# Performance work log

Measured on AMD Instinct MI355X. Metric: run time of the kernel, lower is better.

Reference implementation:

```python
import jax, jax.numpy as jnp
import numpy as np

B, N, D, H, C = 32, 128, 5000, 256, 4  # trees, nodes/tree, input_size_rumor, hidden, rumor_classes


def setup_inputs() -> dict:
    key = jax.random.key(0)
    ks = jax.random.split(key, 24)
    scale = 0.05  # xavier-like scale (module calls init_weight with xavier_uniform_)
    inp = {"x": jax.random.normal(ks[0], (B, N, D), dtype=jnp.float32)}
    names = ["Er", "Wsr_r", "Usr_r", "Wsr_z", "Usr_z", "Wsr_h", "Usr_h",
             "Wr_r", "Ur_r", "Usr2r_r", "Wr_z", "Ur_z", "Usr2r_z",
             "Wr_h", "Ur_h", "Usr2r_h"]
    shapes = [(H, D)] + [(H, H)] * 15
    for i, (n, s) in enumerate(zip(names, shapes)):
        inp[n] = jax.random.normal(ks[i + 1], s, dtype=jnp.float32) * scale
    inp["Vr"] = jax.random.normal(ks[17], (C, H), dtype=jnp.float32) * scale
    inp["br"] = jnp.zeros((C, 1), dtype=jnp.float32)
    # Tree structure: nodes in topological order; slot 0 = zero initial state,
    # node j is stored at slot j+1, parents[:, i] is the SLOT of node i's parent.
    rng = np.random.default_rng(0)
    pslot = np.zeros((B, N), dtype=np.int64)  # root's parent slot = 0 (zeros)
    for i in range(1, N):
        pslot[:, i] = rng.integers(1, i + 1, size=B)  # parent is an earlier node
    has_child = np.zeros((B, N), dtype=bool)
    for i in range(1, N):
        has_child[np.arange(B), pslot[:, i] - 1] = True
    inp["parents"] = jnp.asarray(pslot)
    inp["is_leaf"] = jnp.asarray(~has_child)
    return inp


def _tree_gru(x_tilde, parents, Wsr_r, Usr_r, Wsr_z, Usr_z, Wsr_h, Usr_h,
              Wr_r, Ur_r, Usr2r_r, Wr_z, Ur_z, Usr2r_z, Wr_h, Ur_h, Usr2r_h):
    """x_tilde: [B,N,H] embedded node features; parents: [B,N] parent SLOT ids.
    Returns h_rumor for every node: [B,N,H]. Same math as MultiModel.rumor_forward,
    with the Python recursion replaced by a scan over topologically-ordered nodes,
    vectorized across the batch of trees."""
    Bq, Nq, Hq = x_tilde.shape
    S0 = jnp.zeros((Bq, Nq + 1, Hq), x_tilde.dtype)  # slot 0 = initial zero state

    def step(carry, xs):
        S_sh, S_ru = carry  # [B, N+1, H] stored shared/rumor states
        xt, p, i = xs       # xt: [B,H], p: [B] parent slot, i: node index
        idx = p[:, None, None]
        hsp = jnp.take_along_axis(S_sh, idx, axis=1)[:, 0]  # [B,H] parent shared state
        hrp = jnp.take_along_axis(S_ru, idx, axis=1)[:, 0]  # [B,H] parent rumor state
        # shared GRU cell
        r_sh = jax.nn.sigmoid(xt @ Wsr_r.T + hsp @ Usr_r.T)
        z_sh = jax.nn.sigmoid(xt @ Wsr_z.T + hsp @ Usr_z.T)
        h_sh_t = jnp.tanh(xt @ Wsr_h.T + (hsp * r_sh) @ Usr_h.T)
        h_sh = (1 - z_sh) * hsp + z_sh * h_sh_t
        # rumor GRU cell (conditioned on shared state)
        r_ru = jax.nn.sigmoid(xt @ Wr_r.T + hrp @ Ur_r.T + h_sh @ Usr2r_r.T)
        z_ru = jax.nn.sigmoid(xt @ Wr_z.T + hrp @ Ur_z.T + h_sh @ Usr2r_z.T)
        h_ru_t = jnp.tanh(xt @ Wr_h.T + (hrp * r_ru) @ Ur_h.T + h_sh @ Usr2r_h.T)
        h_ru = (1 - z_ru) * hrp + z_ru * h_ru_t
        S_sh = S_sh.at[:, i + 1, :].set(h_sh)
        S_ru = S_ru.at[:, i + 1, :].set(h_ru)
        return (S_sh, S_ru), None

    xs = (jnp.swapaxes(x_tilde, 0, 1), parents.T, jnp.arange(Nq))
    (S_sh, S_ru), _ = jax.lax.scan(step, (S0, S0), xs)
    return S_ru[:, 1:, :]


def reference(x, Er, Wsr_r, Usr_r, Wsr_z, Usr_z, Wsr_h, Usr_h,
              Wr_r, Ur_r, Usr2r_r, Wr_z, Ur_z, Usr2r_z, Wr_h, Ur_h, Usr2r_h,
              Vr, br, parents, is_leaf):
    x_tilde = jnp.einsum('bnd,hd->bnh', x, Er)  # Er @ x for every node
    H_ru = _tree_gru(x_tilde, parents, Wsr_r, Usr_r, Wsr_z, Usr_z, Wsr_h, Usr_h,
                     Wr_r, Ur_r, Usr2r_r, Wr_z, Ur_z, Usr2r_z, Wr_h, Ur_h, Usr2r_h)
    # max over leaf node hidden vectors (torch.max over cat of leaf vectors)
    neg = jnp.finfo(H_ru.dtype).min
    hmax = jnp.where(is_leaf[:, :, None], H_ru, neg).max(axis=1)  # [B,H]
    logits = hmax @ Vr.T + br[:, 0]  # [B,C]
    return jax.nn.softmax(logits, axis=-1)
```

## Files before the change

### kernel.cpp

```cpp
#include <hip/hip_runtime.h>
#include <hip/hip_bf16.h>
#include <math.h>


#define H_DIM 256
#define N_NODES 128
#define B_TREES 32
#define MAXL 128
#define TPB 4
#define GRID_WGS 256

typedef short bf16x8 __attribute__((ext_vector_type(8)));
typedef float f32x4 __attribute__((ext_vector_type(4)));

__device__ __forceinline__ float sigmoidf_(float x) {
    return 1.0f / (1.0f + expf(-x));
}
__device__ __forceinline__ unsigned bfp(float x) {
    unsigned u = __float_as_uint(x);
    return (u + 0x7fffu + ((u >> 16) & 1u)) >> 16;
}
__device__ __forceinline__ float bflo(unsigned w) { return __uint_as_float(w << 16); }
__device__ __forceinline__ float bfhi(unsigned w) { return __uint_as_float(w & 0xffff0000u); }

__device__ __forceinline__ void unpack8(uint4 v, float* f) {
    f[0] = bflo(v.x); f[1] = bfhi(v.x);
    f[2] = bflo(v.y); f[3] = bfhi(v.y);
    f[4] = bflo(v.z); f[5] = bfhi(v.z);
    f[6] = bflo(v.w); f[7] = bfhi(v.w);
}

__device__ __forceinline__ float coh_load(const float* p) {
    return __hip_atomic_load(p, __ATOMIC_RELAXED, __HIP_MEMORY_SCOPE_AGENT);
}
__device__ __forceinline__ void coh_store(float* p, float v) {
    __hip_atomic_store(p, v, __ATOMIC_RELAXED, __HIP_MEMORY_SCOPE_AGENT);
}
__device__ __forceinline__ unsigned coh_loadu(const unsigned* p) {
    return __hip_atomic_load(p, __ATOMIC_RELAXED, __HIP_MEMORY_SCOPE_AGENT);
}
__device__ __forceinline__ void coh_storeu(unsigned* p, unsigned v) {
    __hip_atomic_store(p, v, __ATOMIC_RELAXED, __HIP_MEMORY_SCOPE_AGENT);
}

__global__ __launch_bounds__(256) void gemm_mfma_nt(
    const float* __restrict__ A, const float* __restrict__ B,
    float* __restrict__ C, int K, int ldc) {
    __shared__ short As[64][40];
    __shared__ short Bs[64][40];
    const int tid = threadIdx.x;
    const int bm = blockIdx.x, bn = blockIdx.y;
    const int row = tid >> 2;
    const int quad = tid & 3;
    const int wave = tid >> 6;
    const int lane = tid & 63;
    const int lm = lane & 15;
    const int kq = lane >> 4;

    f32x4 acc[4];
#pragma unroll
    for (int i = 0; i < 4; ++i) acc[i] = (f32x4){0.f, 0.f, 0.f, 0.f};

    const int nk = (K + 31) >> 5;
    for (int kt = 0; kt < nk; ++kt) {
        const int k0 = kt << 5;
        const int kbase = k0 + quad * 8;
        {
            float a8[8];
            const float* Ap = A + (size_t)(bm * 64 + row) * K + kbase;
            if (kbase + 8 <= K) {
                const float4 v0 = *(const float4*)Ap;
                const float4 v1 = *(const float4*)(Ap + 4);
                a8[0] = v0.x; a8[1] = v0.y; a8[2] = v0.z; a8[3] = v0.w;
                a8[4] = v1.x; a8[5] = v1.y; a8[6] = v1.z; a8[7] = v1.w;
            } else {
#pragma unroll
                for (int i = 0; i < 8; ++i)
                    a8[i] = (kbase + i < K) ? Ap[i] : 0.f;
            }
            uint4 v;
            v.x = bfp(a8[0]) | (bfp(a8[1]) << 16);
            v.y = bfp(a8[2]) | (bfp(a8[3]) << 16);
            v.z = bfp(a8[4]) | (bfp(a8[5]) << 16);
            v.w = bfp(a8[6]) | (bfp(a8[7]) << 16);
            *(uint4*)&As[row][quad * 8] = v;
        }
        {
            float b8[8];
            const float* Bp = B + (size_t)(bn * 64 + row) * K + kbase;
            if (kbase + 8 <= K) {
                const float4 v0 = *(const float4*)Bp;
                const float4 v1 = *(const float4*)(Bp + 4);
                b8[0] = v0.x; b8[1] = v0.y; b8[2] = v0.z; b8[3] = v0.w;
                b8[4] = v1.x; b8[5] = v1.y; b8[6] = v1.z; b8[7] = v1.w;
            } else {
#pragma unroll
                for (int i = 0; i < 8; ++i)
                    b8[i] = (kbase + i < K) ? Bp[i] : 0.f;
            }
            uint4 v;
            v.x = bfp(b8[0]) | (bfp(b8[1]) << 16);
            v.y = bfp(b8[2]) | (bfp(b8[3]) << 16);
            v.z = bfp(b8[4]) | (bfp(b8[5]) << 16);
            v.w = bfp(b8[6]) | (bfp(b8[7]) << 16);
            *(uint4*)&Bs[row][quad * 8] = v;
        }
        __syncthreads();
        const bf16x8 af = *(const bf16x8*)&As[wave * 16 + lm][kq * 8];
#pragma unroll
        for (int nt = 0; nt < 4; ++nt) {
            const bf16x8 bf = *(const bf16x8*)&Bs[nt * 16 + lm][kq * 8];
            acc[nt] = __builtin_amdgcn_mfma_f32_16x16x32_bf16(af, bf, acc[nt], 0, 0, 0);
        }
        __syncthreads();
    }
#pragma unroll
    for (int nt = 0; nt < 4; ++nt) {
#pragma unroll
        for (int r = 0; r < 4; ++r) {
            const int gm = bm * 64 + wave * 16 + kq * 4 + r;
            const int gn = bn * 64 + nt * 16 + lm;
            C[(size_t)gm * ldc + gn] = acc[nt][r];
        }
    }
}

__global__ __launch_bounds__(256) void transpose_pack_u(
    const float* __restrict__ U0, const float* __restrict__ U1,
    const float* __restrict__ U2, const float* __restrict__ U3,
    const float* __restrict__ U4, const float* __restrict__ U5,
    const float* __restrict__ U6, const float* __restrict__ U7,
    const float* __restrict__ U8, uint4* __restrict__ UTb) {
    const float* Us[9] = {U0, U1, U2, U3, U4, U5, U6, U7, U8};
    const int jb = blockIdx.x;
    const int m = blockIdx.y;
    const int h = threadIdx.x;
    const float* U = Us[m] + (size_t)h * 256 + jb * 8;
    uint4 v;
    v.x = bfp(U[0]) | (bfp(U[1]) << 16);
    v.y = bfp(U[2]) | (bfp(U[3]) << 16);
    v.z = bfp(U[4]) | (bfp(U[5]) << 16);
    v.w = bfp(U[6]) | (bfp(U[7]) << 16);
    UTb[(size_t)(m * 32 + jb) * 256 + h] = v;
}

__global__ __launch_bounds__(256) void build_schedule(
    const int* __restrict__ parents, int* __restrict__ sched,
    int* __restrict__ level_off, int* __restrict__ gstart,
    int* __restrict__ gend, int* __restrict__ ngrp,
    unsigned* __restrict__ ready) {
    __shared__ unsigned char depth[B_TREES][N_NODES];
    __shared__ int counts[MAXL];
    __shared__ int base[MAXL + 1];
    const int tid = threadIdx.x;
    for (int k = tid; k < B_TREES * N_NODES; k += 256)
        coh_storeu(&ready[k], 0u);
    for (int k = tid; k < MAXL; k += 256) counts[k] = 0;
    __syncthreads();
    if (tid < B_TREES) {
        depth[tid][0] = 0;
        for (int i = 1; i < N_NODES; ++i) {
            const int p = parents[tid * N_NODES + i];
            depth[tid][i] = (unsigned char)(depth[tid][p - 1] + 1);
        }
    }
    __syncthreads();
    for (int k = tid; k < B_TREES * N_NODES; k += 256)
        atomicAdd(&counts[depth[k >> 7][k & 127]], 1);
    __syncthreads();
    if (tid == 0) {
        int acc = 0;
        int nl = 0;
        for (int l = 0; l < MAXL; ++l) {
            base[l] = acc;
            acc += counts[l];
            if (counts[l] > 0) nl = l + 1;
        }
        base[MAXL] = acc;
        level_off[MAXL + 1] = nl;
        int ng = 0;
        for (int l = 0; l < nl; ++l) {
            for (int s = base[l]; s < base[l + 1]; s += TPB) {
                gstart[ng] = s;
                gend[ng] = (s + TPB < base[l + 1]) ? s + TPB : base[l + 1];
                ++ng;
            }
        }
        *ngrp = ng;
    }
    __syncthreads();
    for (int k = tid; k <= MAXL; k += 256) level_off[k] = base[k];
    for (int k = tid; k < MAXL; k += 256) counts[k] = 0;
    __syncthreads();
    for (int k = tid; k < B_TREES * N_NODES; k += 256) {
        const int d = depth[k >> 7][k & 127];
        const int pos = base[d] + atomicAdd(&counts[d], 1);
        sched[pos] = k;
    }
}

__global__ __launch_bounds__(256, 1) void tree_scan_df(
    const float* __restrict__ P, const uint4* __restrict__ UTb,
    const int* __restrict__ parents,
    const int* __restrict__ sched,
    const int* __restrict__ gstart, const int* __restrict__ gend,
    const int* __restrict__ ngrp, unsigned* __restrict__ ready,
    float* __restrict__ Ssh, float* __restrict__ Sru) {
    const int h = threadIdx.x;
    const int wg = blockIdx.x;
    __shared__ float hsp_s[H_DIM][TPB];
    __shared__ float hrp_s[H_DIM][TPB];
    __shared__ float aux_s[H_DIM][TPB];
    __shared__ float hsh_s[H_DIM][TPB];

    const uint4* __restrict__ U0b = UTb + 0 * 8192;
    const uint4* __restrict__ U1b = UTb + 1 * 8192;
    const uint4* __restrict__ U2b = UTb + 2 * 8192;
    const uint4* __restrict__ U3b = UTb + 3 * 8192;
    const uint4* __restrict__ U4b = UTb + 4 * 8192;
    const uint4* __restrict__ U5b = UTb + 5 * 8192;
    const uint4* __restrict__ U6b = UTb + 6 * 8192;
    const uint4* __restrict__ U7b = UTb + 7 * 8192;
    const uint4* __restrict__ U8b = UTb + 8 * 8192;

    const int ng = ngrp[0];
    for (int g = wg; g < ng; g += GRID_WGS) {
        const int s = gstart[g];
        const int e = gend[g];
        if (h == 0) {
            for (int i = s; i < e; ++i) {
                const int nd = sched[i];
                const int p = parents[nd];
                if (p != 0) {
                    const unsigned* f = &ready[(nd & ~127) + p - 1];
                    while (coh_loadu(f) == 0u) __builtin_amdgcn_s_sleep(2);
                }
            }
        }
        __syncthreads();

        int  node[TPB];
        bool val[TPB];
        float phs[TPB], phr[TPB];
#pragma unroll
        for (int t = 0; t < TPB; ++t) {
            const int idx = s + t;
            val[t] = idx < e;
            const int nd = val[t] ? sched[idx] : sched[s];
            node[t] = nd;
            const int p = parents[nd];
            float hs = 0.f, hr = 0.f;
            if (p != 0) {
                const size_t pr = ((size_t)((nd & ~127) + p - 1)) * H_DIM + h;
                hs = coh_load(&Ssh[pr]);
                hr = coh_load(&Sru[pr]);
            }
            phs[t] = hs;
            phr[t] = hr;
        }
        *(float4*)&hsp_s[h][0] = make_float4(phs[0], phs[1], phs[2], phs[3]);
        *(float4*)&hrp_s[h][0] = make_float4(phr[0], phr[1], phr[2], phr[3]);
        __syncthreads();

        float pr_[TPB], pz_[TPB];
#pragma unroll
        for (int t = 0; t < TPB; ++t) {
            const float* Pi = P + (size_t)node[t] * 1536;
            pr_[t] = Pi[h];
            pz_[t] = Pi[256 + h];
        }
        float dr[TPB] = {0.f, 0.f, 0.f, 0.f};
        float dz[TPB] = {0.f, 0.f, 0.f, 0.f};
#pragma unroll 4
        for (int jb = 0; jb < 32; ++jb) {
            const uint4 w0 = U0b[jb * 256 + h];
            const uint4 w1 = U1b[jb * 256 + h];
            float a[8], c[8];
            unpack8(w0, a);
            unpack8(w1, c);
#pragma unroll
            for (int q = 0; q < 8; ++q) {
                const float4 hv = *(const float4*)&hsp_s[jb * 8 + q][0];
                const float hv4[4] = {hv.x, hv.y, hv.z, hv.w};
#pragma unroll
                for (int t = 0; t < TPB; ++t) {
                    dr[t] = fmaf(a[q], hv4[t], dr[t]);
                    dz[t] = fmaf(c[q], hv4[t], dz[t]);
                }
            }
        }
        float z_sh[TPB], vsh[TPB];
#pragma unroll
        for (int t = 0; t < TPB; ++t) {
            const float r_sh = sigmoidf_(pr_[t] + dr[t]);
            z_sh[t] = sigmoidf_(pz_[t] + dz[t]);
            vsh[t] = phs[t] * r_sh;
        }
        *(float4*)&aux_s[h][0] = make_float4(vsh[0], vsh[1], vsh[2], vsh[3]);
        __syncthreads();

        float ph_[TPB];
#pragma unroll
        for (int t = 0; t < TPB; ++t)
            ph_[t] = P[(size_t)node[t] * 1536 + 512 + h];
        float dh[TPB] = {0.f, 0.f, 0.f, 0.f};
#pragma unroll 8
        for (int jb = 0; jb < 32; ++jb) {
            const uint4 w2 = U2b[jb * 256 + h];
            float a[8];
            unpack8(w2, a);
#pragma unroll
            for (int q = 0; q < 8; ++q) {
                const float4 hv = *(const float4*)&aux_s[jb * 8 + q][0];
                const float hv4[4] = {hv.x, hv.y, hv.z, hv.w};
#pragma unroll
                for (int t = 0; t < TPB; ++t)
                    dh[t] = fmaf(a[q], hv4[t], dh[t]);
            }
        }
        float hsh[TPB];
#pragma unroll
        for (int t = 0; t < TPB; ++t) {
            const float hsh_t = tanhf(ph_[t] + dh[t]);
            hsh[t] = (1.f - z_sh[t]) * phs[t] + z_sh[t] * hsh_t;
            if (val[t])
                coh_store(&Ssh[(size_t)node[t] * H_DIM + h], hsh[t]);
        }
        *(float4*)&hsh_s[h][0] = make_float4(hsh[0], hsh[1], hsh[2], hsh[3]);
        __syncthreads();

        float pru_[TPB], pzu_[TPB];
#pragma unroll
        for (int t = 0; t < TPB; ++t) {
            const float* Pi = P + (size_t)node[t] * 1536;
            pru_[t] = Pi[768 + h];
            pzu_[t] = Pi[1024 + h];
        }
        float er[TPB] = {0.f, 0.f, 0.f, 0.f};
        float ez[TPB] = {0.f, 0.f, 0.f, 0.f};
        float fr[TPB] = {0.f, 0.f, 0.f, 0.f};
        float fz[TPB] = {0.f, 0.f, 0.f, 0.f};
#pragma unroll 2
        for (int jb = 0; jb < 32; ++jb) {
            const uint4 w3 = U3b[jb * 256 + h];
            const uint4 w4 = U4b[jb * 256 + h];
            const uint4 w6 = U6b[jb * 256 + h];
            const uint4 w7 = U7b[jb * 256 + h];
            float a3[8], a4[8], a6[8], a7[8];
            unpack8(w3, a3);
            unpack8(w4, a4);
            unpack8(w6, a6);
            unpack8(w7, a7);
#pragma unroll
            for (int q = 0; q < 8; ++q) {
                const float4 hr4 = *(const float4*)&hrp_s[jb * 8 + q][0];
                const float4 hs4 = *(const float4*)&hsh_s[jb * 8 + q][0];
                const float hrv[4] = {hr4.x, hr4.y, hr4.z, hr4.w};
                const float hsv[4] = {hs4.x, hs4.y, hs4.z, hs4.w};
#pragma unroll
                for (int t = 0; t < TPB; ++t) {
                    er[t] = fmaf(a3[q], hrv[t], er[t]);
                    ez[t] = fmaf(a4[q], hrv[t], ez[t]);
                    fr[t] = fmaf(a6[q], hsv[t], fr[t]);
                    fz[t] = fmaf(a7[q], hsv[t], fz[t]);
                }
            }
        }
        float z_ru[TPB], v2[TPB];
#pragma unroll
        for (int t = 0; t < TPB; ++t) {
            const float r_ru = sigmoidf_(pru_[t] + er[t] + fr[t]);
            z_ru[t] = sigmoidf_(pzu_[t] + ez[t] + fz[t]);
            v2[t] = phr[t] * r_ru;
        }
        *(float4*)&aux_s[h][0] = make_float4(v2[0], v2[1], v2[2], v2[3]);
        __syncthreads();

        float phu_[TPB];
#pragma unroll
        for (int t = 0; t < TPB; ++t)
            phu_[t] = P[(size_t)node[t] * 1536 + 1280 + h];
        float eh[TPB] = {0.f, 0.f, 0.f, 0.f};
        float fh[TPB] = {0.f, 0.f, 0.f, 0.f};
#pragma unroll 4
        for (int jb = 0; jb < 32; ++jb) {
            const uint4 w5 = U5b[jb * 256 + h];
            const uint4 w8 = U8b[jb * 256 + h];
            float a5[8], a8[8];
            unpack8(w5, a5);
            unpack8(w8, a8);
#pragma unroll
            for (int q = 0; q < 8; ++q) {
                const float4 v4 = *(const float4*)&aux_s[jb * 8 + q][0];
                const float4 s4 = *(const float4*)&hsh_s[jb * 8 + q][0];
                const float vv[4] = {v4.x, v4.y, v4.z, v4.w};
                const float sv[4] = {s4.x, s4.y, s4.z, s4.w};
#pragma unroll
                for (int t = 0; t < TPB; ++t) {
                    eh[t] = fmaf(a5[q], vv[t], eh[t]);
                    fh[t] = fmaf(a8[q], sv[t], fh[t]);
                }
            }
        }
#pragma unroll
        for (int t = 0; t < TPB; ++t) {
            const float hru_t = tanhf(phu_[t] + eh[t] + fh[t]);
            const float h_ru = (1.f - z_ru[t]) * phr[t] + z_ru[t] * hru_t;
            if (val[t])
                coh_store(&Sru[(size_t)node[t] * H_DIM + h], h_ru);
        }
        __syncthreads();
        if (h < TPB && s + h < e)
            coh_storeu(&ready[sched[s + h]], 1u);
        __syncthreads();
    }
}

__global__ __launch_bounds__(256) void epilogue_k(
    const float* __restrict__ Sru, const int* __restrict__ is_leaf,
    const float* __restrict__ Vr, const float* __restrict__ br,
    float* __restrict__ out) {
    const int b = blockIdx.x;
    const int h = threadIdx.x;
    float m = -3.402823466e38f;
    for (int n = 0; n < N_NODES; ++n) {
        const float v = Sru[((size_t)b * N_NODES + n) * H_DIM + h];
        if (is_leaf[b * N_NODES + n] != 0) m = fmaxf(m, v);
    }
    __shared__ float hm[H_DIM];
    __shared__ float lg[4];
    hm[h] = m;
    __syncthreads();
    if (h < 4) {
        float acc = br[h];
#pragma unroll 8
        for (int j = 0; j < H_DIM; ++j) acc = fmaf(Vr[h * 256 + j], hm[j], acc);
        lg[h] = acc;
    }
    __syncthreads();
    if (h == 0) {
        const float mx = fmaxf(fmaxf(lg[0], lg[1]), fmaxf(lg[2], lg[3]));
        const float e0 = expf(lg[0] - mx);
        const float e1 = expf(lg[1] - mx);
        const float e2 = expf(lg[2] - mx);
        const float e3 = expf(lg[3] - mx);
        const float s = e0 + e1 + e2 + e3;
        out[b * 4 + 0] = e0 / s;
        out[b * 4 + 1] = e1 / s;
        out[b * 4 + 2] = e2 / s;
        out[b * 4 + 3] = e3 / s;
    }
}

extern "C" void kernel_launch(void* const* d_in, const int* in_sizes, int n_in,
                              void* d_out, int out_size, void* d_ws, size_t ws_size,
                              hipStream_t stream) {
    const float* x      = (const float*)d_in[0];
    const float* Er     = (const float*)d_in[1];
    const float* Wsr_r  = (const float*)d_in[2];
    const float* Usr_r  = (const float*)d_in[3];
    const float* Wsr_z  = (const float*)d_in[4];
    const float* Usr_z  = (const float*)d_in[5];
    const float* Wsr_h  = (const float*)d_in[6];
    const float* Usr_h  = (const float*)d_in[7];
    const float* Wr_r   = (const float*)d_in[8];
    const float* Ur_r   = (const float*)d_in[9];
    const float* Usr2r_r= (const float*)d_in[10];
    const float* Wr_z   = (const float*)d_in[11];
    const float* Ur_z   = (const float*)d_in[12];
    const float* Usr2r_z= (const float*)d_in[13];
    const float* Wr_h   = (const float*)d_in[14];
    const float* Ur_h   = (const float*)d_in[15];
    const float* Usr2r_h= (const float*)d_in[16];
    const float* Vr     = (const float*)d_in[17];
    const float* br     = (const float*)d_in[18];
    const int*   parents= (const int*)d_in[19];
    const int*   is_leaf= (const int*)d_in[20];
    float* out = (float*)d_out;

    float* ws = (float*)d_ws;
    float* xt   = ws;
    float* P    = xt + 1048576;
    float* Wcat = P + 6291456;
    uint4* UTb  = (uint4*)(Wcat + 393216);
    float* Ssh  = (float*)(UTb + 73728);
    float* Sru  = Ssh + 1048576;
    int*   sched     = (int*)(Sru + 1048576);
    int*   level_off = sched + 4096;
    unsigned* ready  = (unsigned*)(level_off + 192);
    int*   gstart    = (int*)(ready + 4096);
    int*   gend      = gstart + 2048;
    int*   ngrp      = gend + 2048;

    dim3 blk(256);

    gemm_mfma_nt<<<dim3(64, 4), blk, 0, stream>>>(x, Er, xt, 5000, 256);

    const float* Ws6[6] = {Wsr_r, Wsr_z, Wsr_h, Wr_r, Wr_z, Wr_h};
    for (int w = 0; w < 6; ++w)
        (void)hipMemcpyAsync(Wcat + (size_t)w * 65536, Ws6[w],
                             65536 * sizeof(float), hipMemcpyDeviceToDevice,
                             stream);
    gemm_mfma_nt<<<dim3(64, 24), blk, 0, stream>>>(xt, Wcat, P, 256, 1536);

    transpose_pack_u<<<dim3(32, 9), blk, 0, stream>>>(
        Usr_r, Usr_z, Usr_h, Ur_r, Ur_z, Ur_h, Usr2r_r, Usr2r_z, Usr2r_h, UTb);

    build_schedule<<<dim3(1), blk, 0, stream>>>(parents, sched, level_off,
                                                gstart, gend, ngrp, ready);

    void* args[] = {(void*)&P, (void*)&UTb, (void*)&parents, (void*)&sched,
                    (void*)&gstart, (void*)&gend, (void*)&ngrp, (void*)&ready,
                    (void*)&Ssh, (void*)&Sru};
    (void)hipLaunchCooperativeKernel((const void*)tree_scan_df,
                                     dim3(GRID_WGS), blk, args, 0, stream);

    epilogue_k<<<dim3(B_TREES), blk, 0, stream>>>(Sru, is_leaf, Vr, br, out);
}
```

Before: 992.0 us.

## Split-K the embedding GEMM, halve nodes per group, parallelize dependency waits

The x·Erᵀ GEMM is split four ways along K (5000), with each slice written to scratch and then summed by a new reduce kernel. This raises the block count from 256 to 1024 on a GEMM that previously ran only 64x4 blocks. The tree scan now packs two nodes per workgroup group instead of four, giving more and smaller groups so the dependency chain is shorter and more parallel. Each node's parent-ready flag is now spun on by its own thread with a shorter sleep. The costs are an extra partial-sum pass through memory and reloading the U weights for fewer nodes per group.

```diff
diff --git a/kernel.cpp b/kernel.cpp
--- a/kernel.cpp
+++ b/kernel.cpp
@@ -7,7 +7,7 @@
 #define N_NODES 128
 #define B_TREES 32
 #define MAXL 128
-#define TPB 4
+#define TPB 2
 #define GRID_WGS 256
 
 typedef short bf16x8 __attribute__((ext_vector_type(8)));
@@ -45,11 +45,15 @@
 
 __global__ __launch_bounds__(256) void gemm_mfma_nt(
     const float* __restrict__ A, const float* __restrict__ B,
-    float* __restrict__ C, int K, int ldc) {
+    float* __restrict__ C, int K, int ldc, int Kc, int zStride) {
     __shared__ short As[64][40];
     __shared__ short Bs[64][40];
     const int tid = threadIdx.x;
     const int bm = blockIdx.x, bn = blockIdx.y;
+    const int z = blockIdx.z;
+    const int k_begin = z * Kc;
+    const int k_end = (k_begin + Kc < K) ? (k_begin + Kc) : K;
+    float* Cz = C + (size_t)z * zStride;
     const int row = tid >> 2;
     const int quad = tid & 3;
     const int wave = tid >> 6;
@@ -61,14 +65,12 @@
 #pragma unroll
     for (int i = 0; i < 4; ++i) acc[i] = (f32x4){0.f, 0.f, 0.f, 0.f};
 
-    const int nk = (K + 31) >> 5;
-    for (int kt = 0; kt < nk; ++kt) {
-        const int k0 = kt << 5;
+    for (int k0 = k_begin; k0 < k_end; k0 += 32) {
         const int kbase = k0 + quad * 8;
         {
             float a8[8];
             const float* Ap = A + (size_t)(bm * 64 + row) * K + kbase;
-            if (kbase + 8 <= K) {
+            if (kbase + 8 <= k_end) {
                 const float4 v0 = *(const float4*)Ap;
                 const float4 v1 = *(const float4*)(Ap + 4);
                 a8[0] = v0.x; a8[1] = v0.y; a8[2] = v0.z; a8[3] = v0.w;
@@ -76,7 +78,7 @@
             } else {
 #pragma unroll
                 for (int i = 0; i < 8; ++i)
-                    a8[i] = (kbase + i < K) ? Ap[i] : 0.f;
+                    a8[i] = (kbase + i < k_end) ? Ap[i] : 0.f;
             }
             uint4 v;
             v.x = bfp(a8[0]) | (bfp(a8[1]) << 16);
@@ -88,7 +90,7 @@
         {
             float b8[8];
             const float* Bp = B + (size_t)(bn * 64 + row) * K + kbase;
-            if (kbase + 8 <= K) {
+            if (kbase + 8 <= k_end) {
                 const float4 v0 = *(const float4*)Bp;
                 const float4 v1 = *(const float4*)(Bp + 4);
                 b8[0] = v0.x; b8[1] = v0.y; b8[2] = v0.z; b8[3] = v0.w;
@@ -96,7 +98,7 @@
             } else {
 #pragma unroll
                 for (int i = 0; i < 8; ++i)
-                    b8[i] = (kbase + i < K) ? Bp[i] : 0.f;
+                    b8[i] = (kbase + i < k_end) ? Bp[i] : 0.f;
             }
             uint4 v;
             v.x = bfp(b8[0]) | (bfp(b8[1]) << 16);
@@ -120,9 +122,24 @@
         for (int r = 0; r < 4; ++r) {
             const int gm = bm * 64 + wave * 16 + kq * 4 + r;
             const int gn = bn * 64 + nt * 16 + lm;
-            C[(size_t)gm * ldc + gn] = acc[nt][r];
-        }
-    }
+            Cz[(size_t)gm * ldc + gn] = acc[nt][r];
+        }
+    }
+}
+
+__global__ __launch_bounds__(256) void reduce4_k(
+    const float* __restrict__ Pp, float* __restrict__ xt) {
+    const int i = (blockIdx.x * 256 + threadIdx.x) * 4;
+    const float4 a = *(const float4*)(Pp + i);
+    const float4 b = *(const float4*)(Pp + 1048576 + i);
+    const float4 c = *(const float4*)(Pp + 2097152 + i);
+    const float4 d = *(const float4*)(Pp + 3145728 + i);
+    float4 s;
+    s.x = a.x + b.x + c.x + d.x;
+    s.y = a.y + b.y + c.y + d.y;
+    s.z = a.z + b.z + c.z + d.z;
+    s.w = a.w + b.w + c.w + d.w;
+    *(float4*)(xt + i) = s;
 }
 
 __global__ __launch_bounds__(256) void transpose_pack_u(
@@ -227,14 +244,12 @@
     for (int g = wg; g < ng; g += GRID_WGS) {
         const int s = gstart[g];
         const int e = gend[g];
-        if (h == 0) {
-            for (int i = s; i < e; ++i) {
-                const int nd = sched[i];
-                const int p = parents[nd];
-                if (p != 0) {
-                    const unsigned* f = &ready[(nd & ~127) + p - 1];
-                    while (coh_loadu(f) == 0u) __builtin_amdgcn_s_sleep(2);
-                }
+        if (h < e - s) {
+            const int nd = sched[s + h];
+            const int p = parents[nd];
+            if (p != 0) {
+                const unsigned* f = &ready[(nd & ~127) + p - 1];
+                while (coh_loadu(f) == 0u) __builtin_amdgcn_s_sleep(1);
             }
         }
         __syncthreads();
@@ -258,8 +273,8 @@
             phs[t] = hs;
             phr[t] = hr;
         }
-        *(float4*)&hsp_s[h][0] = make_float4(phs[0], phs[1], phs[2], phs[3]);
-        *(float4*)&hrp_s[h][0] = make_float4(phr[0], phr[1], phr[2], phr[3]);
+        *(float2*)&hsp_s[h][0] = make_float2(phs[0], phs[1]);
+        *(float2*)&hrp_s[h][0] = make_float2(phr[0], phr[1]);
         __syncthreads();
 
         float pr_[TPB], pz_[TPB];
@@ -269,8 +284,8 @@
             pr_[t] = Pi[h];
             pz_[t] = Pi[256 + h];
         }
-        float dr[TPB] = {0.f, 0.f, 0.f, 0.f};
-        float dz[TPB] = {0.f, 0.f, 0.f, 0.f};
+        float dr[TPB] = {0.f, 0.f};
+        float dz[TPB] = {0.f, 0.f};
 #pragma unroll 4
         for (int jb = 0; jb < 32; ++jb) {
             const uint4 w0 = U0b[jb * 256 + h];
@@ -280,13 +295,11 @@
             unpack8(w1, c);
 #pragma unroll
             for (int q = 0; q < 8; ++q) {
-                const float4 hv = *(const float4*)&hsp_s[jb * 8 + q][0];
-                const float hv4[4] = {hv.x, hv.y, hv.z, hv.w};
-#pragma unroll
-                for (int t = 0; t < TPB; ++t) {
-                    dr[t] = fmaf(a[q], hv4[t], dr[t]);
-                    dz[t] = fmaf(c[q], hv4[t], dz[t]);
-                }
+                const float2 hv = *(const float2*)&hsp_s[jb * 8 + q][0];
+                dr[0] = fmaf(a[q], hv.x, dr[0]);
+                dr[1] = fmaf(a[q], hv.y, dr[1]);
+                dz[0] = fmaf(c[q], hv.x, dz[0]);
+                dz[1] = fmaf(c[q], hv.y, dz[1]);
             }
         }
         float z_sh[TPB], vsh[TPB];
@@ -296,14 +309,14 @@
             z_sh[t] = sigmoidf_(pz_[t] + dz[t]);
             vsh[t] = phs[t] * r_sh;
         }
-        *(float4*)&aux_s[h][0] = make_float4(vsh[0], vsh[1], vsh[2], vsh[3]);
+        *(float2*)&aux_s[h][0] = make_float2(vsh[0], vsh[1]);
         __syncthreads();
 
         float ph_[TPB];
 #pragma unroll
         for (int t = 0; t < TPB; ++t)
             ph_[t] = P[(size_t)node[t] * 1536 + 512 + h];
-        float dh[TPB] = {0.f, 0.f, 0.f, 0.f};
+        float dh[TPB] = {0.f, 0.f};
 #pragma unroll 8
         for (int jb = 0; jb < 32; ++jb) {
             const uint4 w2 = U2b[jb * 256 + h];
@@ -311,11 +324,9 @@
             unpack8(w2, a);
 #pragma unroll
             for (int q = 0; q < 8; ++q) {
-                const float4 hv = *(const float4*)&aux_s[jb * 8 + q][0];
-                const float hv4[4] = {hv.x, hv.y, hv.z, hv.w};
-#pragma unroll
-                for (int t = 0; t < TPB; ++t)
-                    dh[t] = fmaf(a[q], hv4[t], dh[t]);
+                const float2 hv = *(const float2*)&aux_s[jb * 8 + q][0];
+                dh[0] = fmaf(a[q], hv.x, dh[0]);
+                dh[1] = fmaf(a[q], hv.y, dh[1]);
             }
         }
         float hsh[TPB];
@@ -326,7 +337,7 @@
             if (val[t])
                 coh_store(&Ssh[(size_t)node[t] * H_DIM + h], hsh[t]);
         }
-        *(float4*)&hsh_s[h][0] = make_float4(hsh[0], hsh[1], hsh[2], hsh[3]);
+        *(float2*)&hsh_s[h][0] = make_float2(hsh[0], hsh[1]);
         __syncthreads();
 
         float pru_[TPB], pzu_[TPB];
@@ -336,10 +347,10 @@
             pru_[t] = Pi[768 + h];
             pzu_[t] = Pi[1024 + h];
         }
-        float er[TPB] = {0.f, 0.f, 0.f, 0.f};
-        float ez[TPB] = {0.f, 0.f, 0.f, 0.f};
-        float fr[TPB] = {0.f, 0.f, 0.f, 0.f};
-        float fz[TPB] = {0.f, 0.f, 0.f, 0.f};
+        float er[TPB] = {0.f, 0.f};
+        float ez[TPB] = {0.f, 0.f};
+        float fr[TPB] = {0.f, 0.f};
+        float fz[TPB] = {0.f, 0.f};
 #pragma unroll 2
         for (int jb = 0; jb < 32; ++jb) {
             const uint4 w3 = U3b[jb * 256 + h];
@@ -353,17 +364,16 @@
             unpack8(w7, a7);
 #pragma unroll
             for (int q = 0; q < 8; ++q) {
-                const float4 hr4 = *(const float4*)&hrp_s[jb * 8 + q][0];
-                const float4 hs4 = *(const float4*)&hsh_s[jb * 8 + q][0];
-                const float hrv[4] = {hr4.x, hr4.y, hr4.z, hr4.w};
-                const float hsv[4] = {hs4.x, hs4.y, hs4.z, hs4.w};
-#pragma unroll
-                for (int t = 0; t < TPB; ++t) {
-                    er[t] = fmaf(a3[q], hrv[t], er[t]);
-                    ez[t] = fmaf(a4[q], hrv[t], ez[t]);
-                    fr[t] = fmaf(a6[q], hsv[t], fr[t]);
-                    fz[t] = fmaf(a7[q], hsv[t], fz[t]);
-                }
+                const float2 hr2 = *(const float2*)&hrp_s[jb * 8 + q][0];
+                const float2 hs2 = *(const float2*)&hsh_s[jb * 8 + q][0];
+                er[0] = fmaf(a3[q], hr2.x, er[0]);
+                er[1] = fmaf(a3[q], hr2.y, er[1]);
+                ez[0] = fmaf(a4[q], hr2.x, ez[0]);
+                ez[1] = fmaf(a4[q], hr2.y, ez[1]);
+                fr[0] = fmaf(a6[q], hs2.x, fr[0]);
+                fr[1] = fmaf(a6[q], hs2.y, fr[1]);
+                fz[0] = fmaf(a7[q], hs2.x, fz[0]);
+                fz[1] = fmaf(a7[q], hs2.y, fz[1]);
             }
         }
         float z_ru[TPB], v2[TPB];
@@ -373,15 +383,15 @@
             z_ru[t] = sigmoidf_(pzu_[t] + ez[t] + fz[t]);
             v2[t] = phr[t] * r_ru;
         }
-        *(float4*)&aux_s[h][0] = make_float4(v2[0], v2[1], v2[2], v2[3]);
+        *(float2*)&aux_s[h][0] = make_float2(v2[0], v2[1]);
         __syncthreads();
 
         float phu_[TPB];
 #pragma unroll
         for (int t = 0; t < TPB; ++t)
             phu_[t] = P[(size_t)node[t] * 1536 + 1280 + h];
-        float eh[TPB] = {0.f, 0.f, 0.f, 0.f};
-        float fh[TPB] = {0.f, 0.f, 0.f, 0.f};
+        float eh[TPB] = {0.f, 0.f};
+        float fh[TPB] = {0.f, 0.f};
 #pragma unroll 4
         for (int jb = 0; jb < 32; ++jb) {
             const uint4 w5 = U5b[jb * 256 + h];
@@ -391,15 +401,12 @@
             unpack8(w8, a8);
 #pragma unroll
             for (int q = 0; q < 8; ++q) {
-                const float4 v4 = *(const float4*)&aux_s[jb * 8 + q][0];
-                const float4 s4 = *(const float4*)&hsh_s[jb * 8 + q][0];
-                const float vv[4] = {v4.x, v4.y, v4.z, v4.w};
-                const float sv[4] = {s4.x, s4.y, s4.z, s4.w};
-#pragma unroll
-                for (int t = 0; t < TPB; ++t) {
-                    eh[t] = fmaf(a5[q], vv[t], eh[t]);
-                    fh[t] = fmaf(a8[q], sv[t], fh[t]);
-                }
+                const float2 v4 = *(const float2*)&aux_s[jb * 8 + q][0];
+                const float2 s4 = *(const float2*)&hsh_s[jb * 8 + q][0];
+                eh[0] = fmaf(a5[q], v4.x, eh[0]);
+                eh[1] = fmaf(a5[q], v4.y, eh[1]);
+                fh[0] = fmaf(a8[q], s4.x, fh[0]);
+                fh[1] = fmaf(a8[q], s4.y, fh[1]);
             }
         }
 #pragma unroll
@@ -410,7 +417,7 @@
                 coh_store(&Sru[(size_t)node[t] * H_DIM + h], h_ru);
         }
         __syncthreads();
-        if (h < TPB && s + h < e)
+        if (h < e - s)
             coh_storeu(&ready[sched[s + h]], 1u);
         __syncthreads();
     }
@@ -489,19 +496,22 @@
     int*   level_off = sched + 4096;
     unsigned* ready  = (unsigned*)(level_off + 192);
     int*   gstart    = (int*)(ready + 4096);
-    int*   gend      = gstart + 2048;
-    int*   ngrp      = gend + 2048;
+    int*   gend      = gstart + 4096;
+    int*   ngrp      = gend + 4096;
 
     dim3 blk(256);
 
-    gemm_mfma_nt<<<dim3(64, 4), blk, 0, stream>>>(x, Er, xt, 5000, 256);
+    gemm_mfma_nt<<<dim3(64, 4, 4), blk, 0, stream>>>(x, Er, P, 5000, 256,
+                                                     1280, 1048576);
+    reduce4_k<<<dim3(1024), blk, 0, stream>>>(P, xt);
 
     const float* Ws6[6] = {Wsr_r, Wsr_z, Wsr_h, Wr_r, Wr_z, Wr_h};
     for (int w = 0; w < 6; ++w)
         (void)hipMemcpyAsync(Wcat + (size_t)w * 65536, Ws6[w],
                              65536 * sizeof(float), hipMemcpyDeviceToDevice,
                              stream);
-    gemm_mfma_nt<<<dim3(64, 24), blk, 0, stream>>>(xt, Wcat, P, 256, 1536);
+    gemm_mfma_nt<<<dim3(64, 24, 1), blk, 0, stream>>>(xt, Wcat, P, 256, 1536,
+                                                      256, 0);
 
     transpose_pack_u<<<dim3(32, 9), blk, 0, stream>>>(
         Usr_r, Usr_z, Usr_h, Ur_r, Ur_z, Ur_h, Usr2r_r, Usr2r_z, Usr2r_h, UTb);
```

Measured after the change: 822.5 us. 1.21x faster.
